# Optimization experiments

Measured on AMD Instinct MI355X. Metric: run time of the kernel, lower is better.

The kernel has to match this reference:

```python
import jax, jax.numpy as jnp
import numpy as np

B = 256
PROJ_DIM = 512   # blip.projection_dim
MAP_DIM = 512    # map_dim init kwarg
EPS = 1e-12      # F.normalize eps


def setup_inputs() -> dict:
    key = jax.random.key(0)
    ks = jax.random.split(key, 10)
    s_in = 1.0 / np.sqrt(PROJ_DIM)
    s_map = 1.0 / np.sqrt(MAP_DIM)
    s_big = 1.0 / np.sqrt(MAP_DIM * MAP_DIM)
    return {
        "image_embeds": jax.random.normal(ks[0], (B, PROJ_DIM), jnp.float32),
        "text_embeds": jax.random.normal(ks[1], (B, PROJ_DIM), jnp.float32),
        # image_map / text_map Linear(proj_dim -> map_dim)
        "Wi": jax.random.uniform(ks[2], (MAP_DIM, PROJ_DIM), jnp.float32, -s_in, s_in),
        "bi": jax.random.uniform(ks[3], (MAP_DIM,), jnp.float32, -s_in, s_in),
        "Wt": jax.random.uniform(ks[4], (MAP_DIM, PROJ_DIM), jnp.float32, -s_in, s_in),
        "bt": jax.random.uniform(ks[5], (MAP_DIM,), jnp.float32, -s_in, s_in),
        # pre_output Linear(map_dim^2 -> map_dim)
        "Wp": jax.random.uniform(ks[6], (MAP_DIM, MAP_DIM * MAP_DIM), jnp.float32, -s_big, s_big),
        "bp": jax.random.uniform(ks[7], (MAP_DIM,), jnp.float32, -s_big, s_big),
        # classifier Linear(map_dim -> 1)
        "Wc": jax.random.uniform(ks[8], (1, MAP_DIM), jnp.float32, -s_map, s_map),
        "bc": jax.random.uniform(ks[9], (1,), jnp.float32, -s_map, s_map),
    }


def _l2_normalize(x):
    # F.normalize(x, p=2, dim=1): divide by clamped L2 norm
    n = jnp.sqrt(jnp.sum(x * x, axis=1, keepdims=True))
    return x / jnp.maximum(n, EPS)


def reference(image_embeds, text_embeds, Wi, bi, Wt, bt, Wp, bp, Wc, bc):
    # mapping MLPs (dropout = identity at eval)
    img = image_embeds @ Wi.T + bi            # [B, M]
    txt = text_embeds @ Wt.T + bt             # [B, M]
    img = _l2_normalize(img)
    txt = _l2_normalize(txt)
    M = Wi.shape[0]
    # cross head: outer product img_b (x) txt_b flattened (row-major: i*M + j),
    # fed to Linear(M^2 -> M). Fused as a direct bilinear contraction,
    # avoiding the [B, M^2] HBM intermediate:
    # out[b,k] = sum_{i,j} img[b,i] * txt[b,j] * Wp[k, i*M + j]
    feats = jnp.einsum('bi,bj,kij->bk', img, txt, Wp.reshape(M, M, M)) + bp
    feats = jax.nn.relu(feats)
    logits = feats @ Wc.T + bc                # [B, 1]
    return jax.nn.sigmoid(logits)
```

## Files before the change

kernel.cpp:

```cpp
#include <hip/hip_runtime.h>
#include <math.h>

#define BATCH 256
#define D 512
#define WPROW ((size_t)(D * D))
#define BK 128
#define NTILE 64
#define NCHUNK 32

typedef __bf16  bf16x8  __attribute__((ext_vector_type(8)));
typedef float   floatx4 __attribute__((ext_vector_type(4)));

__global__ __launch_bounds__(256)
void map_norm_kernel(const float* __restrict__ img_emb,
                     const float* __restrict__ txt_emb,
                     const float* __restrict__ Wi, const float* __restrict__ bi,
                     const float* __restrict__ Wt, const float* __restrict__ bt,
                     float* __restrict__ imgT,
                     float* __restrict__ txtN)
{
    const int b = blockIdx.x;
    const int is_txt = blockIdx.y;
    const int t = threadIdx.x;
    const float* emb = is_txt ? txt_emb : img_emb;
    const float* W   = is_txt ? Wt : Wi;
    const float* bv  = is_txt ? bt : bi;

    __shared__ float row[D];
    row[t]       = emb[(size_t)b * D + t];
    row[t + 256] = emb[(size_t)b * D + t + 256];
    __syncthreads();

    const int k0 = t, k1 = t + 256;
    float acc0 = bv[k0], acc1 = bv[k1];
    const float4* w0 = (const float4*)(W + (size_t)k0 * D);
    const float4* w1 = (const float4*)(W + (size_t)k1 * D);
    const float4* r4 = (const float4*)row;
#pragma unroll 8
    for (int p = 0; p < D / 4; ++p) {
        float4 rv = r4[p];
        float4 a  = w0[p];
        float4 c  = w1[p];
        acc0 += a.x * rv.x + a.y * rv.y + a.z * rv.z + a.w * rv.w;
        acc1 += c.x * rv.x + c.y * rv.y + c.z * rv.z + c.w * rv.w;
    }

    float ss = acc0 * acc0 + acc1 * acc1;
#pragma unroll
    for (int o = 32; o > 0; o >>= 1) ss += __shfl_down(ss, o);
    __shared__ float red[4];
    if ((t & 63) == 0) red[t >> 6] = ss;
    __syncthreads();
    float total = red[0] + red[1] + red[2] + red[3];
    float inv = 1.0f / fmaxf(sqrtf(total), 1e-12f);
    float v0 = acc0 * inv, v1 = acc1 * inv;

    if (is_txt) {
        txtN[(size_t)b * D + k0] = v0;
        txtN[(size_t)b * D + k1] = v1;
    } else {
        imgT[(size_t)k0 * BATCH + b] = v0;
        imgT[(size_t)k1 * BATCH + b] = v1;
    }
}

__global__ __launch_bounds__(256, 2)
void bilinear_kernel(const float* __restrict__ txtN,
                     const float* __restrict__ imgT,
                     const float* __restrict__ Wp,
                     float* __restrict__ feats)
{
    __shared__ float lds[2][NTILE * BK];

    const int wg   = blockIdx.x;
    const int nt   = wg & 7;
    const int ks   = wg >> 3;
    const int tid  = threadIdx.x;
    const int lane = tid & 63;
    const int wave = tid >> 6;
    const int lane15 = lane & 15;
    const int quad   = lane >> 4;

    const int    n0     = nt * NTILE;
    const size_t kbase0 = (size_t)ks * (NCHUNK * BK);
    const int    i0     = ks * 8;
    const int    brow0  = wave * 64 + lane15;

    const int dma_rowoff = lane >> 5;
    const int dma_bslot  = lane & 31;

    floatx4 acc[4][4];
#pragma unroll
    for (int m = 0; m < 4; ++m)
#pragma unroll
        for (int n = 0; n < 4; ++n) acc[m][n] = (floatx4){0.f, 0.f, 0.f, 0.f};

    auto stage = [&](int cidx, int bufsel) {
        const size_t kb = kbase0 + (size_t)cidx * BK;
#pragma unroll
        for (int u = 0; u < 8; ++u) {
            const int k   = wave * 8 + u;
            const int row = 2 * k + dma_rowoff;
            const int bg  = dma_bslot ^ (row & 7);
            const float* gp = Wp + (size_t)(n0 + row) * WPROW + kb + (size_t)bg * 4;
            float* lp = &lds[bufsel][k * 256];
            __builtin_amdgcn_global_load_lds(
                (__attribute__((address_space(1))) void*)(uintptr_t)gp,
                (__attribute__((address_space(3))) void*)(uintptr_t)lp,
                16, 0, 0);
        }
    };

    stage(0, 0);
    __syncthreads();

    for (int c = 0; c < NCHUNK; ++c) {
        if (c + 1 < NCHUNK) stage(c + 1, (c + 1) & 1);

        const float* buf = lds[c & 1];
        const int i  = i0 + (c >> 2);
        const int jb = (c & 3) * BK;

        float simg[4];
#pragma unroll
        for (int m = 0; m < 4; ++m)
            simg[m] = imgT[(size_t)i * BATCH + brow0 + m * 16];

#pragma unroll
        for (int t = 0; t < 4; ++t) {
            const int j0 = jb + t * 32 + quad * 8;

            float4 ta[4], tb[4];
#pragma unroll
            for (int m = 0; m < 4; ++m) {
                const float4* p =
                    (const float4*)(txtN + (size_t)(brow0 + m * 16) * D + j0);
                ta[m] = p[0];
                tb[m] = p[1];
            }

            bf16x8 bfr[4];
#pragma unroll
            for (int n = 0; n < 4; ++n) {
                const int r  = n * 16 + lane15;
                const int bc = t * 8 + quad * 2;
                const int sw = r & 7;
                const float4 x = *(const float4*)(buf + r * BK + ((bc    ) ^ sw) * 4);
                const float4 y = *(const float4*)(buf + r * BK + ((bc + 1) ^ sw) * 4);
                bf16x8 v;
                v[0] = (__bf16)x.x; v[1] = (__bf16)x.y;
                v[2] = (__bf16)x.z; v[3] = (__bf16)x.w;
                v[4] = (__bf16)y.x; v[5] = (__bf16)y.y;
                v[6] = (__bf16)y.z; v[7] = (__bf16)y.w;
                bfr[n] = v;
            }

#pragma unroll
            for (int m = 0; m < 4; ++m) {
                const float s = simg[m];
                bf16x8 a;
                a[0] = (__bf16)(s * ta[m].x);
                a[1] = (__bf16)(s * ta[m].y);
                a[2] = (__bf16)(s * ta[m].z);
                a[3] = (__bf16)(s * ta[m].w);
                a[4] = (__bf16)(s * tb[m].x);
                a[5] = (__bf16)(s * tb[m].y);
                a[6] = (__bf16)(s * tb[m].z);
                a[7] = (__bf16)(s * tb[m].w);
#pragma unroll
                for (int n = 0; n < 4; ++n)
                    acc[m][n] = __builtin_amdgcn_mfma_f32_16x16x32_bf16(
                        a, bfr[n], acc[m][n], 0, 0, 0);
            }
        }
        __syncthreads();
    }

#pragma unroll
    for (int m = 0; m < 4; ++m)
#pragma unroll
        for (int n = 0; n < 4; ++n)
#pragma unroll
            for (int r = 0; r < 4; ++r) {
                int brow = wave * 64 + m * 16 + quad * 4 + r;
                int kcol = n0 + n * 16 + lane15;
                atomicAdd(&feats[(size_t)brow * D + kcol], acc[m][n][r]);
            }
}

__global__ __launch_bounds__(256)
void epilogue_kernel(const float* __restrict__ feats,
                     const float* __restrict__ bp,
                     const float* __restrict__ Wc,
                     const float* __restrict__ bc,
                     float* __restrict__ out)
{
    const int b = blockIdx.x;
    const int t = threadIdx.x;
    float v0 = fmaxf(feats[(size_t)b * D + t] + bp[t], 0.f) * Wc[t];
    float v1 = fmaxf(feats[(size_t)b * D + t + 256] + bp[t + 256], 0.f) * Wc[t + 256];
    float s = v0 + v1;
#pragma unroll
    for (int o = 32; o > 0; o >>= 1) s += __shfl_down(s, o);
    __shared__ float red[4];
    if ((t & 63) == 0) red[t >> 6] = s;
    __syncthreads();
    if (t == 0) {
        float tot = red[0] + red[1] + red[2] + red[3] + bc[0];
        out[b] = 1.0f / (1.0f + expf(-tot));
    }
}

extern "C" void kernel_launch(void* const* d_in, const int* in_sizes, int n_in,
                              void* d_out, int out_size, void* d_ws, size_t ws_size,
                              hipStream_t stream) {
    const float* image_embeds = (const float*)d_in[0];
    const float* text_embeds  = (const float*)d_in[1];
    const float* Wi = (const float*)d_in[2];
    const float* bi = (const float*)d_in[3];
    const float* Wt = (const float*)d_in[4];
    const float* bt = (const float*)d_in[5];
    const float* Wp = (const float*)d_in[6];
    const float* bp = (const float*)d_in[7];
    const float* Wc = (const float*)d_in[8];
    const float* bc = (const float*)d_in[9];
    float* out = (float*)d_out;

    float* txtN  = (float*)d_ws;
    float* imgT  = txtN + BATCH * D;
    float* feats = imgT + D * BATCH;

    hipMemsetAsync(feats, 0, (size_t)BATCH * D * sizeof(float), stream);
    map_norm_kernel<<<dim3(BATCH, 2), 256, 0, stream>>>(
        image_embeds, text_embeds, Wi, bi, Wt, bt, imgT, txtN);
    bilinear_kernel<<<dim3(512), 256, 0, stream>>>(txtN, imgT, Wp, feats);
    epilogue_kernel<<<dim3(BATCH), 256, 0, stream>>>(feats, bp, Wc, bc, out);
}
```

Baseline: 935.6 us.

## Deepen Wp staging to four-buffer prefetch and reorder loop for txt reuse

Replaces the double-buffered 128-wide Wp chunk pipeline with a four-buffer ring of 64-wide chunks prefetched three ahead, using explicit vmcnt waits and raw barriers instead of __syncthreads. The loop is reordered so j-groups are outer and i inner, letting txtN fragments be held in registers across eight i values, and all eight imgT scalars are hoisted before the loop. The intent is to hide HBM latency on the Wp stream and cut repeated global loads of txt, at the cost of more registers and hand-tuned waitcnt counts that could be fragile.

```diff
diff --git a/kernel.cpp b/kernel.cpp
--- a/kernel.cpp
+++ b/kernel.cpp
@@ -4,9 +4,11 @@
 #define BATCH 256
 #define D 512
 #define WPROW ((size_t)(D * D))
-#define BK 128
 #define NTILE 64
-#define NCHUNK 32
+#define BK 64
+#define NCHUNK 64
+#define NBUF 4
+#define PFD 3
 
 typedef __bf16  bf16x8  __attribute__((ext_vector_type(8)));
 typedef float   floatx4 __attribute__((ext_vector_type(4)));
@@ -70,7 +72,7 @@
                      const float* __restrict__ Wp,
                      float* __restrict__ feats)
 {
-    __shared__ float lds[2][NTILE * BK];
+    __shared__ float lds[NBUF][NTILE * BK];
 
     const int wg   = blockIdx.x;
     const int nt   = wg & 7;
@@ -81,13 +83,12 @@
     const int lane15 = lane & 15;
     const int quad   = lane >> 4;
 
-    const int    n0     = nt * NTILE;
-    const size_t kbase0 = (size_t)ks * (NCHUNK * BK);
-    const int    i0     = ks * 8;
-    const int    brow0  = wave * 64 + lane15;
-
-    const int dma_rowoff = lane >> 5;
-    const int dma_bslot  = lane & 31;
+    const int n0    = nt * NTILE;
+    const int i0    = ks * 8;
+    const int brow0 = wave * 64 + lane15;
+
+    const int dma_rowoff = lane >> 4;
+    const int dma_slot   = lane & 15;
 
     floatx4 acc[4][4];
 #pragma unroll
@@ -95,15 +96,36 @@
 #pragma unroll
         for (int n = 0; n < 4; ++n) acc[m][n] = (floatx4){0.f, 0.f, 0.f, 0.f};
 
-    auto stage = [&](int cidx, int bufsel) {
-        const size_t kb = kbase0 + (size_t)cidx * BK;
-#pragma unroll
-        for (int u = 0; u < 8; ++u) {
-            const int k   = wave * 8 + u;
-            const int row = 2 * k + dma_rowoff;
-            const int bg  = dma_bslot ^ (row & 7);
-            const float* gp = Wp + (size_t)(n0 + row) * WPROW + kb + (size_t)bg * 4;
-            float* lp = &lds[bufsel][k * 256];
+    float simg[8][4];
+#pragma unroll
+    for (int il = 0; il < 8; ++il)
+#pragma unroll
+        for (int m = 0; m < 4; ++m)
+            simg[il][m] = imgT[(size_t)(i0 + il) * BATCH + brow0 + m * 16];
+
+    float4 ta[2][4][2];
+    auto refresh = [&](int jg) {
+#pragma unroll
+        for (int t = 0; t < 2; ++t)
+#pragma unroll
+            for (int m = 0; m < 4; ++m) {
+                const float4* p = (const float4*)(txtN +
+                    (size_t)(brow0 + m * 16) * D + jg * 64 + t * 32 + quad * 8);
+                ta[t][m][0] = p[0];
+                ta[t][m][1] = p[1];
+            }
+    };
+
+    auto stage = [&](int c) {
+        const int    bufs = c & (NBUF - 1);
+        const size_t kb   = (size_t)(i0 + (c & 7)) * D + (size_t)(c >> 3) * BK;
+#pragma unroll
+        for (int u = 0; u < 4; ++u) {
+            const int rbase = wave * 16 + u * 4;
+            const int row   = rbase + dma_rowoff;
+            const int slot  = dma_slot ^ (row & 7);
+            const float* gp = Wp + (size_t)(n0 + row) * WPROW + kb + slot * 4;
+            float* lp = &lds[bufs][rbase * BK];
             __builtin_amdgcn_global_load_lds(
                 (__attribute__((address_space(1))) void*)(uintptr_t)gp,
                 (__attribute__((address_space(3))) void*)(uintptr_t)lp,
@@ -111,69 +133,64 @@
         }
     };
 
-    stage(0, 0);
-    __syncthreads();
-
-    for (int c = 0; c < NCHUNK; ++c) {
-        if (c + 1 < NCHUNK) stage(c + 1, (c + 1) & 1);
-
-        const float* buf = lds[c & 1];
-        const int i  = i0 + (c >> 2);
-        const int jb = (c & 3) * BK;
-
-        float simg[4];
-#pragma unroll
-        for (int m = 0; m < 4; ++m)
-            simg[m] = imgT[(size_t)i * BATCH + brow0 + m * 16];
-
-#pragma unroll
-        for (int t = 0; t < 4; ++t) {
-            const int j0 = jb + t * 32 + quad * 8;
-
-            float4 ta[4], tb[4];
-#pragma unroll
-            for (int m = 0; m < 4; ++m) {
-                const float4* p =
-                    (const float4*)(txtN + (size_t)(brow0 + m * 16) * D + j0);
-                ta[m] = p[0];
-                tb[m] = p[1];
-            }
-
-            bf16x8 bfr[4];
-#pragma unroll
-            for (int n = 0; n < 4; ++n) {
-                const int r  = n * 16 + lane15;
+    refresh(0);
+    stage(0); stage(1); stage(2);
+
+#pragma unroll 1
+    for (int g = 0; g < 8; ++g) {
+#pragma unroll
+        for (int il = 0; il < 8; ++il) {
+            const int c = g * 8 + il;
+
+            if (il <= 5) {
+                asm volatile("s_waitcnt vmcnt(8)" ::: "memory");
+            } else if (il == 6) {
+                if (g == 7) asm volatile("s_waitcnt vmcnt(4)" ::: "memory");
+                else        asm volatile("s_waitcnt vmcnt(8)" ::: "memory");
+            } else {
+                if (g == 7) asm volatile("s_waitcnt vmcnt(0)" ::: "memory");
+                else        asm volatile("s_waitcnt vmcnt(8)" ::: "memory");
+            }
+            __builtin_amdgcn_s_barrier();
+            asm volatile("" ::: "memory");
+
+            if (il == 0 && g > 0) refresh(g);
+            if (c + PFD < NCHUNK) stage(c + PFD);
+
+            const float* Bt = &lds[c & (NBUF - 1)][0];
+#pragma unroll
+            for (int t = 0; t < 2; ++t) {
                 const int bc = t * 8 + quad * 2;
-                const int sw = r & 7;
-                const float4 x = *(const float4*)(buf + r * BK + ((bc    ) ^ sw) * 4);
-                const float4 y = *(const float4*)(buf + r * BK + ((bc + 1) ^ sw) * 4);
-                bf16x8 v;
-                v[0] = (__bf16)x.x; v[1] = (__bf16)x.y;
-                v[2] = (__bf16)x.z; v[3] = (__bf16)x.w;
-                v[4] = (__bf16)y.x; v[5] = (__bf16)y.y;
-                v[6] = (__bf16)y.z; v[7] = (__bf16)y.w;
-                bfr[n] = v;
-            }
-
-#pragma unroll
-            for (int m = 0; m < 4; ++m) {
-                const float s = simg[m];
-                bf16x8 a;
-                a[0] = (__bf16)(s * ta[m].x);
-                a[1] = (__bf16)(s * ta[m].y);
-                a[2] = (__bf16)(s * ta[m].z);
-                a[3] = (__bf16)(s * ta[m].w);
-                a[4] = (__bf16)(s * tb[m].x);
-                a[5] = (__bf16)(s * tb[m].y);
-                a[6] = (__bf16)(s * tb[m].z);
-                a[7] = (__bf16)(s * tb[m].w);
-#pragma unroll
-                for (int n = 0; n < 4; ++n)
-                    acc[m][n] = __builtin_amdgcn_mfma_f32_16x16x32_bf16(
-                        a, bfr[n], acc[m][n], 0, 0, 0);
+                bf16x8 bfr[4];
+#pragma unroll
+                for (int n = 0; n < 4; ++n) {
+                    const int r  = n * 16 + lane15;
+                    const int sw = r & 7;
+                    const float4 x = *(const float4*)(Bt + r * BK + ((bc    ) ^ sw) * 4);
+                    const float4 y = *(const float4*)(Bt + r * BK + ((bc + 1) ^ sw) * 4);
+                    bf16x8 v;
+                    v[0] = (__bf16)x.x; v[1] = (__bf16)x.y;
+                    v[2] = (__bf16)x.z; v[3] = (__bf16)x.w;
+                    v[4] = (__bf16)y.x; v[5] = (__bf16)y.y;
+                    v[6] = (__bf16)y.z; v[7] = (__bf16)y.w;
+                    bfr[n] = v;
+                }
+#pragma unroll
+                for (int m = 0; m < 4; ++m) {
+                    const float  s  = simg[il][m];
+                    const float4 u0 = ta[t][m][0], u1 = ta[t][m][1];
+                    bf16x8 a;
+                    a[0] = (__bf16)(s * u0.x); a[1] = (__bf16)(s * u0.y);
+                    a[2] = (__bf16)(s * u0.z); a[3] = (__bf16)(s * u0.w);
+                    a[4] = (__bf16)(s * u1.x); a[5] = (__bf16)(s * u1.y);
+                    a[6] = (__bf16)(s * u1.z); a[7] = (__bf16)(s * u1.w);
+#pragma unroll
+                    for (int n = 0; n < 4; ++n)
+                        acc[m][n] = __builtin_amdgcn_mfma_f32_16x16x32_bf16(
+                            a, bfr[n], acc[m][n], 0, 0, 0);
+                }
             }
         }
-        __syncthreads();
     }
 
 #pragma unroll
```

Result: faster. 909.5 us (-2.8%).

## Factor image scale out of bilinear MFMA and keep text fragments in registers

Applied to the files above, without the earlier changes.

The bilinear kernel is restructured so each workgroup handles 16 output columns and 16 image indices. Text fragments are converted to bf16 once and held in registers, and the per-image scalar is applied after each MFMA chunk rather than before it, which removes the repeated per-chunk scaling and global reloads of text. Weight tiles move through a triple-buffered LDS pipeline with explicit vmcnt waits, and the grid doubles to 1024 workgroups. The cost is heavier register pressure from the 32 cached fragments, and each workgroup now reads a narrower weight tile.

```diff
diff --git a/kernel.cpp b/kernel.cpp
--- a/kernel.cpp
+++ b/kernel.cpp
@@ -4,8 +4,9 @@
 #define BATCH 256
 #define D 512
 #define WPROW ((size_t)(D * D))
-#define BK 128
-#define NTILE 64
+#define NTILE 16
+#define NI    16
+#define NBUF  3
 #define NCHUNK 32
 
 typedef __bf16  bf16x8  __attribute__((ext_vector_type(8)));
@@ -70,40 +71,54 @@
                      const float* __restrict__ Wp,
                      float* __restrict__ feats)
 {
-    __shared__ float lds[2][NTILE * BK];
+    __shared__ float wbuf[NBUF][NTILE * 256];
+    __shared__ float simgL[NI * BATCH];
 
     const int wg   = blockIdx.x;
-    const int nt   = wg & 7;
-    const int ks   = wg >> 3;
+    const int nt   = wg & 31;
+    const int ks   = wg >> 5;
     const int tid  = threadIdx.x;
     const int lane = tid & 63;
     const int wave = tid >> 6;
     const int lane15 = lane & 15;
     const int quad   = lane >> 4;
 
-    const int    n0     = nt * NTILE;
-    const size_t kbase0 = (size_t)ks * (NCHUNK * BK);
-    const int    i0     = ks * 8;
-    const int    brow0  = wave * 64 + lane15;
-
-    const int dma_rowoff = lane >> 5;
-    const int dma_bslot  = lane & 31;
-
-    floatx4 acc[4][4];
-#pragma unroll
-    for (int m = 0; m < 4; ++m)
-#pragma unroll
-        for (int n = 0; n < 4; ++n) acc[m][n] = (floatx4){0.f, 0.f, 0.f, 0.f};
-
-    auto stage = [&](int cidx, int bufsel) {
-        const size_t kb = kbase0 + (size_t)cidx * BK;
-#pragma unroll
-        for (int u = 0; u < 8; ++u) {
-            const int k   = wave * 8 + u;
-            const int row = 2 * k + dma_rowoff;
-            const int bg  = dma_bslot ^ (row & 7);
-            const float* gp = Wp + (size_t)(n0 + row) * WPROW + kb + (size_t)bg * 4;
-            float* lp = &lds[bufsel][k * 256];
+    const int n0    = nt * NTILE;
+    const int i0    = ks * NI;
+    const int brow0 = wave * 64 + lane15;
+
+    floatx4 acc[4];
+#pragma unroll
+    for (int m = 0; m < 4; ++m) acc[m] = (floatx4){0.f, 0.f, 0.f, 0.f};
+
+    bf16x8 afr[4][8];
+    auto loadA = [&](int jh) {
+#pragma unroll
+        for (int m = 0; m < 4; ++m)
+#pragma unroll
+            for (int k8 = 0; k8 < 8; ++k8) {
+                const float4* p = (const float4*)(txtN +
+                    (size_t)(brow0 + m * 16) * D + jh * 256 + k8 * 32 + quad * 8);
+                float4 u0 = p[0], u1 = p[1];
+                bf16x8 a;
+                a[0] = (__bf16)u0.x; a[1] = (__bf16)u0.y;
+                a[2] = (__bf16)u0.z; a[3] = (__bf16)u0.w;
+                a[4] = (__bf16)u1.x; a[5] = (__bf16)u1.y;
+                a[6] = (__bf16)u1.z; a[7] = (__bf16)u1.w;
+                afr[m][k8] = a;
+            }
+    };
+
+    auto stage = [&](int c, int buf) {
+        const int    i       = c & 15;
+        const int    jh      = c >> 4;
+        const size_t colbase = (size_t)(i0 + i) * D + jh * 256;
+#pragma unroll
+        for (int u = 0; u < 4; ++u) {
+            const int r     = wave * 4 + u;
+            const int gslot = lane ^ (r & 7);
+            const float* gp = Wp + (size_t)(n0 + r) * WPROW + colbase + gslot * 4;
+            float* lp = &wbuf[buf][r * 256];
             __builtin_amdgcn_global_load_lds(
                 (__attribute__((address_space(1))) void*)(uintptr_t)gp,
                 (__attribute__((address_space(3))) void*)(uintptr_t)lp,
@@ -111,81 +126,74 @@
         }
     };
 
+    loadA(0);
+#pragma unroll
+    for (int i = 0; i < NI; ++i)
+        simgL[i * BATCH + tid] = imgT[(size_t)(i0 + i) * BATCH + tid];
+    __syncthreads();
+
     stage(0, 0);
-    __syncthreads();
-
+    stage(1, 1);
+
+    int bcur = 0;
+#pragma unroll 1
     for (int c = 0; c < NCHUNK; ++c) {
-        if (c + 1 < NCHUNK) stage(c + 1, (c + 1) & 1);
-
-        const float* buf = lds[c & 1];
-        const int i  = i0 + (c >> 2);
-        const int jb = (c & 3) * BK;
-
-        float simg[4];
-#pragma unroll
-        for (int m = 0; m < 4; ++m)
-            simg[m] = imgT[(size_t)i * BATCH + brow0 + m * 16];
-
-#pragma unroll
-        for (int t = 0; t < 4; ++t) {
-            const int j0 = jb + t * 32 + quad * 8;
-
-            float4 ta[4], tb[4];
-#pragma unroll
-            for (int m = 0; m < 4; ++m) {
-                const float4* p =
-                    (const float4*)(txtN + (size_t)(brow0 + m * 16) * D + j0);
-                ta[m] = p[0];
-                tb[m] = p[1];
-            }
-
-            bf16x8 bfr[4];
-#pragma unroll
-            for (int n = 0; n < 4; ++n) {
-                const int r  = n * 16 + lane15;
-                const int bc = t * 8 + quad * 2;
-                const int sw = r & 7;
-                const float4 x = *(const float4*)(buf + r * BK + ((bc    ) ^ sw) * 4);
-                const float4 y = *(const float4*)(buf + r * BK + ((bc + 1) ^ sw) * 4);
-                bf16x8 v;
-                v[0] = (__bf16)x.x; v[1] = (__bf16)x.y;
-                v[2] = (__bf16)x.z; v[3] = (__bf16)x.w;
-                v[4] = (__bf16)y.x; v[5] = (__bf16)y.y;
-                v[6] = (__bf16)y.z; v[7] = (__bf16)y.w;
-                bfr[n] = v;
-            }
-
-#pragma unroll
-            for (int m = 0; m < 4; ++m) {
-                const float s = simg[m];
-                bf16x8 a;
-                a[0] = (__bf16)(s * ta[m].x);
-                a[1] = (__bf16)(s * ta[m].y);
-                a[2] = (__bf16)(s * ta[m].z);
-                a[3] = (__bf16)(s * ta[m].w);
-                a[4] = (__bf16)(s * tb[m].x);
-                a[5] = (__bf16)(s * tb[m].y);
-                a[6] = (__bf16)(s * tb[m].z);
-                a[7] = (__bf16)(s * tb[m].w);
-#pragma unroll
-                for (int n = 0; n < 4; ++n)
-                    acc[m][n] = __builtin_amdgcn_mfma_f32_16x16x32_bf16(
-                        a, bfr[n], acc[m][n], 0, 0, 0);
-            }
-        }
-        __syncthreads();
+        if (c < NCHUNK - 1) asm volatile("s_waitcnt vmcnt(4)" ::: "memory");
+        else                asm volatile("s_waitcnt vmcnt(0)" ::: "memory");
+        __builtin_amdgcn_s_barrier();
+        asm volatile("" ::: "memory");
+
+        if (c == 16) loadA(1);
+        if (c + 2 < NCHUNK) {
+            int b2 = bcur + 2; if (b2 >= NBUF) b2 -= NBUF;
+            stage(c + 2, b2);
+        }
+
+        const float* Bt = &wbuf[bcur][0];
+        floatx4 cacc[4];
+#pragma unroll
+        for (int m = 0; m < 4; ++m) cacc[m] = (floatx4){0.f, 0.f, 0.f, 0.f};
+
+#pragma unroll
+        for (int k8 = 0; k8 < 8; ++k8) {
+            const int r  = lane15;
+            const int sw = r & 7;
+            const int s6 = k8 * 8 + quad * 2;
+            const float4 x = *(const float4*)(Bt + r * 256 + ((s6    ) ^ sw) * 4);
+            const float4 y = *(const float4*)(Bt + r * 256 + ((s6 + 1) ^ sw) * 4);
+            bf16x8 b;
+            b[0] = (__bf16)x.x; b[1] = (__bf16)x.y;
+            b[2] = (__bf16)x.z; b[3] = (__bf16)x.w;
+            b[4] = (__bf16)y.x; b[5] = (__bf16)y.y;
+            b[6] = (__bf16)y.z; b[7] = (__bf16)y.w;
+#pragma unroll
+            for (int m = 0; m < 4; ++m)
+                cacc[m] = __builtin_amdgcn_mfma_f32_16x16x32_bf16(
+                    afr[m][k8], b, cacc[m], 0, 0, 0);
+        }
+
+        const int ci = c & 15;
+#pragma unroll
+        for (int m = 0; m < 4; ++m) {
+            const float4 sc = *(const float4*)(
+                &simgL[ci * BATCH + wave * 64 + m * 16 + quad * 4]);
+            acc[m][0] += sc.x * cacc[m][0];
+            acc[m][1] += sc.y * cacc[m][1];
+            acc[m][2] += sc.z * cacc[m][2];
+            acc[m][3] += sc.w * cacc[m][3];
+        }
+
+        ++bcur; if (bcur == NBUF) bcur = 0;
     }
 
 #pragma unroll
     for (int m = 0; m < 4; ++m)
 #pragma unroll
-        for (int n = 0; n < 4; ++n)
-#pragma unroll
-            for (int r = 0; r < 4; ++r) {
-                int brow = wave * 64 + m * 16 + quad * 4 + r;
-                int kcol = n0 + n * 16 + lane15;
-                atomicAdd(&feats[(size_t)brow * D + kcol], acc[m][n][r]);
-            }
+        for (int r = 0; r < 4; ++r) {
+            int brow = wave * 64 + m * 16 + quad * 4 + r;
+            int kcol = n0 + lane15;
+            atomicAdd(&feats[(size_t)brow * D + kcol], acc[m][r]);
+        }
 }
 
 __global__ __launch_bounds__(256)
@@ -233,6 +241,6 @@
     hipMemsetAsync(feats, 0, (size_t)BATCH * D * sizeof(float), stream);
     map_norm_kernel<<<dim3(BATCH, 2), 256, 0, stream>>>(
         image_embeds, text_embeds, Wi, bi, Wt, bt, imgT, txtN);
-    bilinear_kernel<<<dim3(512), 256, 0, stream>>>(txtN, imgT, Wp, feats);
+    bilinear_kernel<<<dim3(1024), 256, 0, stream>>>(txtN, imgT, Wp, feats);
     epilogue_kernel<<<dim3(BATCH), 256, 0, stream>>>(feats, bp, Wc, bc, out);
 }
```

Measured after the change: 792.7 us. -15.3%, faster.
